# Kernel optimization log

Hardware: AMD Instinct MI355X
Metric: run time of the kernel (lower is better)

## Reference

```python
import jax, jax.numpy as jnp
import numpy as np


def setup_inputs() -> dict:
    key = jax.random.key(0)
    k1, k2 = jax.random.split(key)
    N, F, E = 100000, 128, 600000
    x = jax.random.normal(k1, (N, F), dtype=jnp.float32)
    edge_index = jax.random.randint(k2, (2, E), 0, N, dtype=jnp.int64)
    return {"x": x, "edge_index": edge_index}


def reference(x, edge_index):
    # x: [N, F] node features; edge_index: [2, E]
    ei = edge_index.T  # [E, 2]
    N = x.shape[0]
    E = ei.shape[0]

    # Midpoint node insertion: mean of the two endpoint features per edge.
    mid = 0.5 * (x[ei[:, 0]] + x[ei[:, 1]])  # [E, F]
    new_x = jnp.concatenate([x, mid], axis=0)  # [N+E, F]

    # New node indices N .. N+E-1
    new_idx = jnp.arange(N, N + E)
    e1 = jnp.stack([ei[:, 0], new_idx], axis=1)  # src -> midpoint
    e2 = jnp.stack([new_idx, ei[:, 1]], axis=1)  # midpoint -> dst

    # Triangle edges among consecutive triples of new nodes (vectorized form
    # of the original Python loop: for i in range(N, N+E-2, 3)).
    T = -(-(E - 2) // 3) if E > 2 else 0  # ceil((E-2)/3) == number of loop iters
    i = N + 3 * jnp.arange(T)
    tri = jnp.stack([i, i + 1, i + 1, i + 2, i + 2, i], axis=1).reshape(-1, 2)  # [3T, 2]

    new_ei = jnp.concatenate([ei, e1, e2, tri], axis=0)  # [E + 2E + 3T, 2]
    return new_x, new_ei.T
```

## Files before the change

kernel.cpp:

```cpp
#include <hip/hip_runtime.h>


#define F 128
#define F4 32
#define BSHIFT 10
#define SLOTS 8192
#define SPB_BLOCKS (SLOTS / 16)
#define CHUNK 2048

typedef float f32x4 __attribute__((ext_vector_type(4)));
typedef unsigned long long u64;

__device__ __forceinline__ void nt_store4(f32x4 v, f32x4* p) {
    asm volatile("global_store_dwordx4 %0, %1, off sc0 sc1 nt"
                 :: "v"(p), "v"(v) : "memory");
}
__device__ __forceinline__ void nt_store1(float v, float* p) {
    asm volatile("global_store_dword %0, %1, off sc0 sc1 nt"
                 :: "v"(p), "v"(v) : "memory");
}

__global__ void init_kernel(int* __restrict__ cursor, int NB) {
    const int t = threadIdx.x;
    if (t < NB) cursor[t] = t * SLOTS;
}

__global__ __launch_bounds__(256) void scatter_kernel(
        const int* __restrict__ ei0, const int* __restrict__ ei1,
        int* __restrict__ cursor, u64* __restrict__ tup, int E, int NB) {
    __shared__ int lh[128];
    __shared__ int lbase[128];
    const int t = threadIdx.x;
    if (t < 128) lh[t] = 0;
    __syncthreads();
    const int base = blockIdx.x * CHUNK;
    int s[8], d[8], bk[8], rk[8];
#pragma unroll
    for (int i = 0; i < 8; ++i) {
        const int e = base + i * 256 + t;
        if (e < E) {
            s[i] = ei0[e];
            d[i] = ei1[e];
            bk[i] = s[i] >> BSHIFT;
            rk[i] = atomicAdd(&lh[bk[i]], 1);
        } else {
            bk[i] = -1;
        }
    }
    __syncthreads();
    if (t < NB) {
        const int c = lh[t];
        lbase[t] = c ? atomicAdd(&cursor[t], c) : 0;
    }
    __syncthreads();
#pragma unroll
    for (int i = 0; i < 8; ++i) {
        if (bk[i] >= 0) {
            const int e = base + i * 256 + t;
            const int pos = lbase[bk[i]] + rk[i];
            if (pos < (bk[i] + 1) * SLOTS) {
                const u64 pk = (u64)(e | ((s[i] & 1023) << 20));
                tup[pos] = (pk << 32) | (unsigned)d[i];
            }
        }
    }
}

__global__ __launch_bounds__(256) void main_kernel(
        const f32x4* __restrict__ x4,
        const int* __restrict__ ei0, const int* __restrict__ ei1,
        const u64* __restrict__ tup, const int* __restrict__ cursor,
        f32x4* __restrict__ out4, float* __restrict__ r0, float* __restrict__ r1,
        int N, int E, int M, int NB, int MB, int EBlk) {
    const unsigned b = blockIdx.x;

    if (b < (unsigned)MB) {
        const int xcd = b & 7;
        const int seq = b >> 3;
        const int bucket = xcd + 8 * (seq / SPB_BLOCKS);
        if (bucket >= NB) return;
        const int cnt = cursor[bucket] - bucket * SLOTS;
        const int chunk = seq % SPB_BLOCKS;
        const int si0 = chunk * 16 + (threadIdx.x >> 5) * 2;
        if (si0 >= cnt) return;
        const int lane = threadIdx.x & 31;
        const int p0 = bucket * SLOTS + si0;
        const int nbase = bucket << BSHIFT;

        const u64 t0 = tup[p0];
        const bool have1 = (si0 + 1) < cnt;
        const u64 t1 = have1 ? tup[p0 + 1] : 0;

        const int d0 = (int)(t0 & 0xffffffffu);
        const int pk0 = (int)(t0 >> 32);
        const int s0 = nbase | (pk0 >> 20);
        const int e0 = pk0 & 0xFFFFF;

        f32x4 a0 = x4[(size_t)s0 * F4 + lane];
        f32x4 b0 = x4[(size_t)d0 * F4 + lane];

        if (have1) {
            const int d1 = (int)(t1 & 0xffffffffu);
            const int pk1 = (int)(t1 >> 32);
            const int s1 = nbase | (pk1 >> 20);
            const int e1 = pk1 & 0xFFFFF;
            f32x4 a1 = x4[(size_t)s1 * F4 + lane];
            f32x4 b1 = x4[(size_t)d1 * F4 + lane];
            nt_store4(0.5f * (a0 + b0), &out4[(size_t)(N + e0) * F4 + lane]);
            nt_store4(0.5f * (a1 + b1), &out4[(size_t)(N + e1) * F4 + lane]);
        } else {
            nt_store4(0.5f * (a0 + b0), &out4[(size_t)(N + e0) * F4 + lane]);
        }
        return;
    }

    const unsigned eb = b - MB;
    if (eb < (unsigned)EBlk) {
        const int col = eb * 256 + threadIdx.x;
        if (col >= M) return;
        int a, c;
        if (col < E) {
            a = ei0[col];
            c = ei1[col];
        } else if (col < 2 * E) {
            const int e = col - E;
            a = ei0[e];
            c = N + e;
        } else if (col < 3 * E) {
            const int e = col - 2 * E;
            a = N + e;
            c = ei1[e];
        } else {
            const int j = col - 3 * E;
            const int tt = j / 3;
            const int k = j - 3 * tt;
            const int i = N + 3 * tt;
            a = i + k;
            c = (k < 2) ? (i + k + 1) : i;
        }
        nt_store1((float)a, &r0[col]);
        nt_store1((float)c, &r1[col]);
        return;
    }

    const unsigned cb = eb - EBlk;
    const int lane = threadIdx.x & 31;
    const int g = threadIdx.x >> 5;
    const long long row0 = (long long)cb * 16 + g * 2;
    if (row0 < N) {
        f32x4 v0 = x4[row0 * F4 + lane];
        nt_store4(v0, &out4[row0 * F4 + lane]);
    }
    const long long row1 = row0 + 1;
    if (row1 < N) {
        f32x4 v1 = x4[row1 * F4 + lane];
        nt_store4(v1, &out4[row1 * F4 + lane]);
    }
}

extern "C" void kernel_launch(void* const* d_in, const int* in_sizes, int n_in,
                              void* d_out, int out_size, void* d_ws, size_t ws_size,
                              hipStream_t stream) {
    const float* x = (const float*)d_in[0];
    const int* ei = (const int*)d_in[1];

    const int N = in_sizes[0] / F;
    const int E = in_sizes[1] / 2;
    const int T = (E > 2) ? (E - 2 + 2) / 3 : 0;
    const int M = 3 * E + 3 * T;

    const int* ei0 = ei;
    const int* ei1 = ei + E;

    float* out = (float*)d_out;
    float* r0 = out + (size_t)(N + E) * F;
    float* r1 = r0 + M;

    int* cursor = (int*)d_ws;
    u64* tup = (u64*)((char*)d_ws + 4096);

    const int NB = (N + (1 << BSHIFT) - 1) >> BSHIFT;
    const int NBpad = (NB + 7) & ~7;
    const int MB = NBpad * SPB_BLOCKS;
    const int EBlk = (M + 255) / 256;
    const int CB = (N + 15) / 16;

    init_kernel<<<1, 128, 0, stream>>>(cursor, NB);
    scatter_kernel<<<(E + CHUNK - 1) / CHUNK, 256, 0, stream>>>(
        ei0, ei1, cursor, tup, E, NB);
    main_kernel<<<MB + EBlk + CB, 256, 0, stream>>>(
        (const f32x4*)x, ei0, ei1, tup, cursor, (f32x4*)out, r0, r1,
        N, E, M, NB, MB, EBlk);
}
```

Baseline: 133.7 us.

## Fuse edge-index output into scatter kernel and co-schedule copy blocks per bucket

Writing of the output edge-index rows (original, src->mid, mid->dst, triangle edges) moves into the scatter kernel, which already loads ei0/ei1. This removes the re-read of the indices and the separate edge blocks from the main kernel. The main kernel now assigns 64 copy blocks per bucket next to that bucket's 512 midpoint blocks, so the x rows of a bucket are copied on the same XCD that gathers from them, which should improve L2 reuse. The scatter kernel gets more stores, so its latency rises, and the triangle writes depend on the scatter grid covering 3T indices.

```diff
diff --git a/kernel.cpp b/kernel.cpp
--- a/kernel.cpp
+++ b/kernel.cpp
@@ -5,7 +5,9 @@
 #define F4 32
 #define BSHIFT 10
 #define SLOTS 8192
-#define SPB_BLOCKS (SLOTS / 16)
+#define SPB 512
+#define CPB 64
+#define BPB (SPB + CPB)
 #define CHUNK 2048
 
 typedef float f32x4 __attribute__((ext_vector_type(4)));
@@ -27,7 +29,9 @@
 
 __global__ __launch_bounds__(256) void scatter_kernel(
         const int* __restrict__ ei0, const int* __restrict__ ei1,
-        int* __restrict__ cursor, u64* __restrict__ tup, int E, int NB) {
+        int* __restrict__ cursor, u64* __restrict__ tup,
+        float* __restrict__ r0, float* __restrict__ r1,
+        int N, int E, int TT3, int NB) {
     __shared__ int lh[128];
     __shared__ int lbase[128];
     const int t = threadIdx.x;
@@ -43,8 +47,22 @@
             d[i] = ei1[e];
             bk[i] = s[i] >> BSHIFT;
             rk[i] = atomicAdd(&lh[bk[i]], 1);
+            const float fs = (float)s[i], fd = (float)d[i], fm = (float)(N + e);
+            nt_store1(fs, &r0[e]);
+            nt_store1(fd, &r1[e]);
+            nt_store1(fs, &r0[E + e]);
+            nt_store1(fm, &r1[E + e]);
+            nt_store1(fm, &r0[2 * E + e]);
+            nt_store1(fd, &r1[2 * E + e]);
         } else {
             bk[i] = -1;
+        }
+        if (e < TT3) {
+            const int tt = e / 3;
+            const int k = e - 3 * tt;
+            const int ii = N + 3 * tt;
+            nt_store1((float)(ii + k), &r0[3 * E + e]);
+            nt_store1((float)((k < 2) ? (ii + k + 1) : ii), &r1[3 * E + e]);
         }
     }
     __syncthreads();
@@ -68,22 +86,23 @@
 
 __global__ __launch_bounds__(256) void main_kernel(
         const f32x4* __restrict__ x4,
-        const int* __restrict__ ei0, const int* __restrict__ ei1,
         const u64* __restrict__ tup, const int* __restrict__ cursor,
-        f32x4* __restrict__ out4, float* __restrict__ r0, float* __restrict__ r1,
-        int N, int E, int M, int NB, int MB, int EBlk) {
+        f32x4* __restrict__ out4,
+        int N, int NB, int MBlk) {
     const unsigned b = blockIdx.x;
+    if (b >= (unsigned)MBlk) return;
+    const int xcd = b & 7;
+    const int seq = b >> 3;
+    const int bucket = xcd + 8 * (seq / BPB);
+    if (bucket >= NB) return;
+    const int r = seq % BPB;
+    const int lane = threadIdx.x & 31;
+    const int g = threadIdx.x >> 5;
 
-    if (b < (unsigned)MB) {
-        const int xcd = b & 7;
-        const int seq = b >> 3;
-        const int bucket = xcd + 8 * (seq / SPB_BLOCKS);
-        if (bucket >= NB) return;
+    if (r < SPB) {
         const int cnt = cursor[bucket] - bucket * SLOTS;
-        const int chunk = seq % SPB_BLOCKS;
-        const int si0 = chunk * 16 + (threadIdx.x >> 5) * 2;
+        const int si0 = r * 16 + g * 2;
         if (si0 >= cnt) return;
-        const int lane = threadIdx.x & 31;
         const int p0 = bucket * SLOTS + si0;
         const int nbase = bucket << BSHIFT;
 
@@ -111,50 +130,18 @@
         } else {
             nt_store4(0.5f * (a0 + b0), &out4[(size_t)(N + e0) * F4 + lane]);
         }
-        return;
-    }
-
-    const unsigned eb = b - MB;
-    if (eb < (unsigned)EBlk) {
-        const int col = eb * 256 + threadIdx.x;
-        if (col >= M) return;
-        int a, c;
-        if (col < E) {
-            a = ei0[col];
-            c = ei1[col];
-        } else if (col < 2 * E) {
-            const int e = col - E;
-            a = ei0[e];
-            c = N + e;
-        } else if (col < 3 * E) {
-            const int e = col - 2 * E;
-            a = N + e;
-            c = ei1[e];
-        } else {
-            const int j = col - 3 * E;
-            const int tt = j / 3;
-            const int k = j - 3 * tt;
-            const int i = N + 3 * tt;
-            a = i + k;
-            c = (k < 2) ? (i + k + 1) : i;
+    } else {
+        const int cr = r - SPB;
+        const long long row0 = ((long long)bucket << BSHIFT) + cr * 16 + g * 2;
+        if (row0 < N) {
+            f32x4 v0 = x4[row0 * F4 + lane];
+            nt_store4(v0, &out4[row0 * F4 + lane]);
         }
-        nt_store1((float)a, &r0[col]);
-        nt_store1((float)c, &r1[col]);
-        return;
-    }
-
-    const unsigned cb = eb - EBlk;
-    const int lane = threadIdx.x & 31;
-    const int g = threadIdx.x >> 5;
-    const long long row0 = (long long)cb * 16 + g * 2;
-    if (row0 < N) {
-        f32x4 v0 = x4[row0 * F4 + lane];
-        nt_store4(v0, &out4[row0 * F4 + lane]);
-    }
-    const long long row1 = row0 + 1;
-    if (row1 < N) {
-        f32x4 v1 = x4[row1 * F4 + lane];
-        nt_store4(v1, &out4[row1 * F4 + lane]);
+        const long long row1 = row0 + 1;
+        if (row1 < N) {
+            f32x4 v1 = x4[row1 * F4 + lane];
+            nt_store4(v1, &out4[row1 * F4 + lane]);
+        }
     }
 }
 
@@ -181,14 +168,11 @@
 
     const int NB = (N + (1 << BSHIFT) - 1) >> BSHIFT;
     const int NBpad = (NB + 7) & ~7;
-    const int MB = NBpad * SPB_BLOCKS;
-    const int EBlk = (M + 255) / 256;
-    const int CB = (N + 15) / 16;
+    const int MBlk = NBpad * BPB;
 
     init_kernel<<<1, 128, 0, stream>>>(cursor, NB);
     scatter_kernel<<<(E + CHUNK - 1) / CHUNK, 256, 0, stream>>>(
-        ei0, ei1, cursor, tup, E, NB);
-    main_kernel<<<MB + EBlk + CB, 256, 0, stream>>>(
-        (const f32x4*)x, ei0, ei1, tup, cursor, (f32x4*)out, r0, r1,
-        N, E, M, NB, MB, EBlk);
+        ei0, ei1, cursor, tup, r0, r1, N, E, 3 * T, NB);
+    main_kernel<<<MBlk, 256, 0, stream>>>(
+        (const f32x4*)x, tup, cursor, (f32x4*)out, N, NB, MBlk);
 }
```

New measurement: 126.8 us, median of 2. 1.05x faster.
